# Performance work log

Hardware: AMD Instinct MI355X
Metric: run time of the kernel (lower is better)

## Reference

```python
import jax, jax.numpy as jnp
import numpy as np

ALPHA = 0.2
BETA = 1.0
TEMPERATURE = 0.05
EPS = 1e-8  # torch cosine_similarity eps


def setup_inputs() -> dict:
    key = jax.random.key(0)
    k1, k2 = jax.random.split(key)
    B, R, D = 4096, 18, 256  # rows, segment size (1 anchor + 1 pos + 16 negs), embed dim
    features = jax.random.normal(k1, (B * R, D), dtype=jnp.float32)
    scores = jax.random.normal(k2, (B * (R - 1),), dtype=jnp.float32)
    row_sizes = jnp.full((B,), R, dtype=jnp.int32)  # uniform ragged sizes
    logit_scale = jnp.array([1.0 / TEMPERATURE], dtype=jnp.float32)
    return {"features": features, "scores": scores, "row_sizes": row_sizes,
            "logit_scale": logit_scale}


def reference(features, scores, row_sizes, logit_scale):
    B = row_sizes.shape[0]
    R = features.shape[0] // B  # uniform segment size
    D = features.shape[1]
    f3 = features.reshape(B, R, D)
    anchor = f3[:, 0]          # [B, D]
    tgt = f3[:, 1:]            # [B, R-1, D]  (positive first, then negatives)

    # --- per-row cosine sims + log_softmax + KLDiv(batchmean) ---
    an = jnp.maximum(jnp.linalg.norm(anchor, axis=-1, keepdims=True), EPS)  # [B,1]
    tn = jnp.maximum(jnp.linalg.norm(tgt, axis=-1), EPS)                    # [B,R-1]
    cos = jnp.einsum('bd,bkd->bk', anchor, tgt) / (an * tn)                 # [B,R-1]
    emb_log = jax.nn.log_softmax(cos, axis=-1)                              # [B,R-1]
    ce = jax.nn.softmax(scores.reshape(B, R - 1), axis=-1)                  # [B,R-1]
    # torch KLDivLoss(reduction='batchmean') on a length-(R-1) vector divides by (R-1)
    kl = jnp.sum(ce * (jnp.log(ce) - emb_log), axis=-1) / (R - 1)           # [B]
    loss = jnp.mean(BETA * kl)

    # --- single InfoNCE over all rows: anchors vs [positives; all negatives] ---
    pos = f3[:, 1]                                   # [B, D]
    negs = f3[:, 2:].reshape(B * (R - 2), D)         # [B*(R-2), D]
    targets = jnp.concatenate([pos, negs], axis=0)   # [B*(R-1), D]
    logits = logit_scale[0] * (anchor @ targets.T)   # [B, B*(R-1)]
    labels = jnp.arange(B)
    # cross_entropy(logits, labels) with mean reduction
    infonce = jnp.mean(jax.nn.logsumexp(logits, axis=-1) - logits[labels, labels])

    return loss + ALPHA * infonce
```

## Files before the change

### kernel.cpp

```cpp
#include <hip/hip_runtime.h>
#include <math.h>

#define ALPHA 0.2f
#define BETA 1.0f
#define EPSV 1e-8f
#define LOG2E 1.4426950408889634f
#define LN2 0.6931471805599453f

#define BATCH 4096
#define RR 18
#define KT 17
#define DD 256
#define NTGT (BATCH*KT)
#define NTILE (NTGT/32)
#define TILE_BYTES (32*DD)

#define AG 16
#define NSPLIT 32
#define TPS (NTILE/NSPLIT)
#define NRING 4

#define EXPA 8388608.0f
#define EXPB 1064880320.0f

typedef int   i32x8  __attribute__((ext_vector_type(8)));
typedef float f32x16 __attribute__((ext_vector_type(16)));

__device__ inline void gl_lds16(const void* g, void* l){
  __builtin_amdgcn_global_load_lds(
      (const __attribute__((address_space(1))) unsigned int*)g,
      (__attribute__((address_space(3))) unsigned int*)l, 16, 0, 0);
}

__device__ inline int pk8(float a, float b, float c, float d){
  int p = __builtin_amdgcn_cvt_pk_fp8_f32(a, b, 0, false);
  return  __builtin_amdgcn_cvt_pk_fp8_f32(c, d, p, true);
}

__device__ inline float fmax3(float a, float b, float c){
  return fmaxf(fmaxf(a, b), c);
}

__device__ inline float fexp2u(float x, float kc){
  float t = fmaf(x, EXPA, kc);
  unsigned u;
  asm("v_cvt_u32_f32 %0, %1" : "=v"(u) : "v"(t));
  return __uint_as_float(u);
}


__global__ __launch_bounds__(256) void prep_kernel(
    const float* __restrict__ feat, const float* __restrict__ scores,
    const float* __restrict__ lscale,
    unsigned char* __restrict__ abf8, unsigned char* __restrict__ tbf8,
    float* __restrict__ diag, float* __restrict__ klarr,
    float* __restrict__ out){
  __shared__ float csh[KT];
  int b = blockIdx.x, tid = threadIdx.x;
  int grp = tid >> 4, j = tid & 15;
  const float* fb = feat + (size_t)b * RR * DD;
  float s2 = lscale[0] * LOG2E;

  if (b == 0 && tid == 0) out[0] = 0.f;

  float4 a0 = ((const float4*)fb)[j*4+0];
  float4 a1 = ((const float4*)fb)[j*4+1];
  float4 a2 = ((const float4*)fb)[j*4+2];
  float4 a3 = ((const float4*)fb)[j*4+3];
  float asq = (a0.x*a0.x+a0.y*a0.y+a0.z*a0.z+a0.w*a0.w)
            + (a1.x*a1.x+a1.y*a1.y+a1.z*a1.z+a1.w*a1.w)
            + (a2.x*a2.x+a2.y*a2.y+a2.z*a2.z+a2.w*a2.w)
            + (a3.x*a3.x+a3.y*a3.y+a3.z*a3.z+a3.w*a3.w);
  #pragma unroll
  for (int off=1; off<16; off<<=1) asq += __shfl_xor(asq, off);
  float an = fmaxf(sqrtf(asq), EPSV);

  if (tid < 16){
    uint4 v = make_uint4(
      (unsigned)pk8(a0.x*s2,a0.y*s2,a0.z*s2,a0.w*s2),
      (unsigned)pk8(a1.x*s2,a1.y*s2,a1.z*s2,a1.w*s2),
      (unsigned)pk8(a2.x*s2,a2.y*s2,a2.z*s2,a2.w*s2),
      (unsigned)pk8(a3.x*s2,a3.y*s2,a3.z*s2,a3.w*s2));
    *(uint4*)(abf8 + (size_t)b*DD + j*16) = v;
  }

  for (int kr = grp+1; kr <= KT; kr += 16){
    const float4* tp = (const float4*)(fb + (size_t)kr*DD) + j*4;
    float4 t0=tp[0], t1=tp[1], t2=tp[2], t3=tp[3];
    int t  = b*KT + (kr-1);
    int tile = t >> 5, m = t & 31;
    int ki = j >> 2, hf = (j >> 1) & 1, w = j & 1;
    uint4 v = make_uint4(
      (unsigned)pk8(t0.x,t0.y,t0.z,t0.w), (unsigned)pk8(t1.x,t1.y,t1.z,t1.w),
      (unsigned)pk8(t2.x,t2.y,t2.z,t2.w), (unsigned)pk8(t3.x,t3.y,t3.z,t3.w));
    *(uint4*)(tbf8 + (size_t)tile*TILE_BYTES + ki*2048 + w*1024 + hf*512 + m*16) = v;
    float d = (a0.x*t0.x+a0.y*t0.y+a0.z*t0.z+a0.w*t0.w)
            + (a1.x*t1.x+a1.y*t1.y+a1.z*t1.z+a1.w*t1.w)
            + (a2.x*t2.x+a2.y*t2.y+a2.z*t2.z+a2.w*t2.w)
            + (a3.x*t3.x+a3.y*t3.y+a3.z*t3.z+a3.w*t3.w);
    float q = (t0.x*t0.x+t0.y*t0.y+t0.z*t0.z+t0.w*t0.w)
            + (t1.x*t1.x+t1.y*t1.y+t1.z*t1.z+t1.w*t1.w)
            + (t2.x*t2.x+t2.y*t2.y+t2.z*t2.z+t2.w*t2.w)
            + (t3.x*t3.x+t3.y*t3.y+t3.z*t3.z+t3.w*t3.w);
    #pragma unroll
    for (int off=1; off<16; off<<=1){ d += __shfl_xor(d,off); q += __shfl_xor(q,off); }
    if (j == 0){
      csh[kr-1] = d / (an * fmaxf(sqrtf(q), EPSV));
      if (kr == 1) diag[b] = d;
    }
  }
  __syncthreads();

  if (tid < 64){
    bool act = tid < KT;
    float c  = act ? csh[tid] : -INFINITY;
    float sv = act ? scores[(size_t)b*KT + tid] : -INFINITY;
    float cm = c, sm = sv;
    #pragma unroll
    for (int off=1; off<64; off<<=1){
      cm = fmaxf(cm, __shfl_xor(cm, off));
      sm = fmaxf(sm, __shfl_xor(sm, off));
    }
    float ec = act ? __builtin_amdgcn_exp2f((c -cm)*LOG2E) : 0.f;
    float es = act ? __builtin_amdgcn_exp2f((sv-sm)*LOG2E) : 0.f;
    float cs = ec, ss = es;
    #pragma unroll
    for (int off=1; off<64; off<<=1){
      cs += __shfl_xor(cs, off);
      ss += __shfl_xor(ss, off);
    }
    float lse_c = cm + __logf(cs);
    float lse_s = sm + __logf(ss);
    float kt = 0.f;
    if (act){
      float lq = sv - lse_s;
      float lp = c  - lse_c;
      kt = __builtin_amdgcn_exp2f(lq*LOG2E)*(lq - lp);
    }
    #pragma unroll
    for (int off=1; off<64; off<<=1) kt += __shfl_xor(kt, off);
    if (tid == 0) klarr[b] = kt * (1.0f/KT);
  }
}

__global__ __launch_bounds__(256,2) void gemm_lse_kernel(
    const unsigned char* __restrict__ abf8, const unsigned char* __restrict__ tbf8,
    float* __restrict__ part_m, float* __restrict__ part_s){
  __shared__ __align__(16) unsigned char Bs[NRING][TILE_BYTES];
  const int bid  = blockIdx.x;
  const int ns   = (bid & 7)*4 + ((bid >> 3) & 3);
  const int ag   = bid >> 5;
  const int tid  = threadIdx.x;
  const int lane = tid & 63;
  const int wave = tid >> 6;
  const int l31  = lane & 31;
  const int half = lane >> 5;

  const unsigned char* gbase = tbf8 + (size_t)(ns*TPS)*TILE_BYTES;
  auto stage = [&](int t){
    const unsigned char* g = gbase + (size_t)t*TILE_BYTES;
    unsigned char* l = &Bs[t & (NRING-1)][0];
    #pragma unroll
    for (int jj=0;jj<2;++jj){
      int off = jj*4096 + tid*16;
      gl_lds16(g + off, l + off);
    }
  };

  stage(0);
  stage(1);

  i32x8 af[2][4];
  {
    const unsigned char* ab = abf8 + (size_t)(ag*256 + wave*64)*DD;
    #pragma unroll
    for (int nt=0;nt<2;++nt)
      #pragma unroll
      for (int ki=0;ki<4;++ki){
        const unsigned char* p = ab + (size_t)(nt*32+l31)*DD + ki*64 + half*32;
        uint4 lo = *(const uint4*)p;
        uint4 hi = *(const uint4*)(p+16);
        af[nt][ki] = (i32x8){(int)lo.x,(int)lo.y,(int)lo.z,(int)lo.w,
                             (int)hi.x,(int)hi.y,(int)hi.z,(int)hi.w};
      }
  }

  float run_m[2] = {-INFINITY,-INFINITY};
  float run_s[2] = {0.f,0.f};
  f32x16 accA[2], accB[2];
  #pragma unroll
  for (int nt=0;nt<2;++nt){ accA[nt]=(f32x16)(0.f); accB[nt]=(f32x16)(0.f); }

  auto mfma_tile = [&](int t, f32x16 (&acc)[2], bool last){
    if (last) asm volatile("s_waitcnt vmcnt(0)" ::: "memory");
    else      asm volatile("s_waitcnt vmcnt(2)" ::: "memory");
    __builtin_amdgcn_s_barrier();
    asm volatile("" ::: "memory");
    if (t+2 < TPS) stage(t+2);

    const unsigned char* fb = &Bs[t & (NRING-1)][0] + half*512 + l31*16;
    i32x8 tf[4];
    #pragma unroll
    for (int ki=0;ki<4;++ki){
      uint4 lo = *(const uint4*)(fb + ki*2048);
      uint4 hi = *(const uint4*)(fb + ki*2048 + 1024);
      tf[ki] = (i32x8){(int)lo.x,(int)lo.y,(int)lo.z,(int)lo.w,
                       (int)hi.x,(int)hi.y,(int)hi.z,(int)hi.w};
    }
    __builtin_amdgcn_s_setprio(1);
    #pragma unroll
    for (int ki=0;ki<4;++ki){
      acc[0] = __builtin_amdgcn_mfma_scale_f32_32x32x64_f8f6f4(
                   tf[ki], af[0][ki], acc[0], 0,0, 0,127, 0,127);
      acc[1] = __builtin_amdgcn_mfma_scale_f32_32x32x64_f8f6f4(
                   tf[ki], af[1][ki], acc[1], 0,0, 0,127, 0,127);
    }
    __builtin_amdgcn_s_setprio(0);
  };

  auto epilogue = [&](f32x16 (&acc)[2]){
    #pragma unroll
    for (int nt=0;nt<2;++nt){
      f32x16 t = acc[nt];
      float x0 = fmax3(t[0], t[1], t[2]);
      float x1 = fmax3(t[3], t[4], t[5]);
      float x2 = fmax3(t[6], t[7], t[8]);
      float x3 = fmax3(t[9], t[10], t[11]);
      float x4 = fmax3(t[12], t[13], t[14]);
      float mx = fmaxf(fmax3(x0,x1,x2), fmax3(x3,x4,t[15]));

      float kc = fmaf(mx, -EXPA, EXPB);
      float s0=0.f, s1=0.f, s2=0.f, s3=0.f;
      #pragma unroll
      for (int r=0;r<16;r+=4){
        s0 += fexp2u(t[r  ],kc);
        s1 += fexp2u(t[r+1],kc);
        s2 += fexp2u(t[r+2],kc);
        s3 += fexp2u(t[r+3],kc);
      }
      float sh = (s0+s1)+(s2+s3);

      float nm = fmaxf(run_m[nt], mx);
      run_s[nt] = run_s[nt]*__builtin_amdgcn_exp2f(run_m[nt]-nm)
                + sh*__builtin_amdgcn_exp2f(mx-nm);
      run_m[nt] = nm;
      acc[nt] = (f32x16)(0.f);
    }
  };

  mfma_tile(0, accA, false);
  for (int t=1; t+1 < TPS; t+=2){
    mfma_tile(t,   accB, false);
    epilogue(accA);
    mfma_tile(t+1, accA, false);
    epilogue(accB);
  }
  mfma_tile(TPS-1, accB, true);
  epilogue(accA);
  epilogue(accB);

  #pragma unroll
  for (int nt=0;nt<2;++nt){
    float om = __shfl_xor(run_m[nt], 32);
    float os = __shfl_xor(run_s[nt], 32);
    float nm = fmaxf(run_m[nt], om);
    float S  = run_s[nt]*__builtin_amdgcn_exp2f(run_m[nt]-nm)
             + os*__builtin_amdgcn_exp2f(om-nm);
    if (half == 0){
      int gm = ag*256 + wave*64 + nt*32 + l31;
      part_m[(size_t)ns*BATCH + gm] = nm;
      part_s[(size_t)ns*BATCH + gm] = S;
    }
  }
}

__global__ __launch_bounds__(256) void combine_kernel(
    const float* __restrict__ part_m, const float* __restrict__ part_s,
    const float* __restrict__ diag, const float* __restrict__ klarr,
    const float* __restrict__ lscale, float* __restrict__ out){
  int tid = threadIdx.x;
  int b = blockIdx.x*256 + tid;
  float s = lscale[0];
  float m = -INFINITY, S = 0.f;
  #pragma unroll
  for (int ns=0; ns<NSPLIT; ++ns){
    float pm_ = part_m[(size_t)ns*BATCH + b];
    float ps_ = part_s[(size_t)ns*BATCH + b];
    float nm = fmaxf(m, pm_);
    S = S*__builtin_amdgcn_exp2f(m-nm) + ps_*__builtin_amdgcn_exp2f(pm_-nm);
    m = nm;
  }
  float inf = (m + __log2f(S))*LN2 - s*diag[b];
  float c = BETA*klarr[b] + ALPHA*inf;
  #pragma unroll
  for (int off=1; off<64; off<<=1) c += __shfl_xor(c, off);
  if ((tid & 63) == 0) atomicAdd(out, c*(1.0f/BATCH));
}

extern "C" void kernel_launch(void* const* d_in, const int* in_sizes, int n_in,
                              void* d_out, int out_size, void* d_ws, size_t ws_size,
                              hipStream_t stream){
  const float* feat   = (const float*)d_in[0];
  const float* scores = (const float*)d_in[1];
  const float* lscale = (const float*)d_in[3];

  float* ws     = (float*)d_ws;
  float* diag   = ws;
  float* klarr  = diag + BATCH;
  float* part_m = klarr + BATCH;
  float* part_s = part_m + (size_t)NSPLIT*BATCH;
  unsigned char* abf8 = (unsigned char*)(part_s + (size_t)NSPLIT*BATCH);
  unsigned char* tbf8 = abf8 + (size_t)BATCH*DD;

  float* outp = (float*)d_out;
  prep_kernel<<<BATCH, 256, 0, stream>>>(feat, scores, lscale, abf8, tbf8,
                                         diag, klarr, outp);
  gemm_lse_kernel<<<AG*NSPLIT, 256, 0, stream>>>(abf8, tbf8, part_m, part_s);
  combine_kernel<<<BATCH/256, 256, 0, stream>>>(part_m, part_s, diag, klarr,
                                                lscale, outp);
}
```

Measured before the change: 188.0 us.

## Double-tile phases with deeper LDS ring and interleaved MFMA/exp scheduling

Restructures the GEMM+LSE main loop to process two tiles per barrier phase with an 8-deep LDS ring, halving barriers and prefetching two phases ahead. Uses sched_group_barrier to interleave the epilogue VALU work with the MFMAs. The exp-bit trick now uses packed FMA, and the online-softmax update uses a single exp2 with a select. This raises LDS usage and relies on the compiler honouring the schedule hints.

```diff
diff --git a/kernel.cpp b/kernel.cpp
--- a/kernel.cpp
+++ b/kernel.cpp
@@ -18,13 +18,17 @@
 #define AG 16
 #define NSPLIT 32
 #define TPS (NTILE/NSPLIT)
-#define NRING 4
+#define PHASES (TPS/2)
+#define NRING 8
 
 #define EXPA 8388608.0f
 #define EXPB 1064880320.0f
 
 typedef int   i32x8  __attribute__((ext_vector_type(8)));
 typedef float f32x16 __attribute__((ext_vector_type(16)));
+typedef float f32x2  __attribute__((ext_vector_type(2)));
+
+#define SGB __builtin_amdgcn_sched_group_barrier
 
 __device__ inline void gl_lds16(const void* g, void* l){
   __builtin_amdgcn_global_load_lds(
@@ -41,10 +45,15 @@
   return fmaxf(fmaxf(a, b), c);
 }
 
-__device__ inline float fexp2u(float x, float kc){
-  float t = fmaf(x, EXPA, kc);
+__device__ inline f32x2 pk_fma2(f32x2 a, f32x2 b, f32x2 c){
+  f32x2 d;
+  asm("v_pk_fma_f32 %0, %1, %2, %3" : "=v"(d) : "v"(a), "v"(b), "v"(c));
+  return d;
+}
+
+__device__ inline float cvtbit(float x){
   unsigned u;
-  asm("v_cvt_u32_f32 %0, %1" : "=v"(u) : "v"(t));
+  asm("v_cvt_u32_f32 %0, %1" : "=v"(u) : "v"(x));
   return __uint_as_float(u);
 }
 
@@ -157,18 +166,16 @@
   const int half = lane >> 5;
 
   const unsigned char* gbase = tbf8 + (size_t)(ns*TPS)*TILE_BYTES;
-  auto stage = [&](int t){
+  auto stage_tile = [&](int t){
     const unsigned char* g = gbase + (size_t)t*TILE_BYTES;
     unsigned char* l = &Bs[t & (NRING-1)][0];
-    #pragma unroll
-    for (int jj=0;jj<2;++jj){
-      int off = jj*4096 + tid*16;
-      gl_lds16(g + off, l + off);
-    }
+    gl_lds16(g + tid*16,        l + tid*16);
+    gl_lds16(g + 4096 + tid*16, l + 4096 + tid*16);
   };
-
-  stage(0);
-  stage(1);
+  auto stage_phase = [&](int p){ stage_tile(2*p); stage_tile(2*p+1); };
+
+  stage_phase(0);
+  stage_phase(1);
 
   i32x8 af[2][4];
   {
@@ -188,16 +195,9 @@
   float run_m[2] = {-INFINITY,-INFINITY};
   float run_s[2] = {0.f,0.f};
   f32x16 accA[2], accB[2];
-  #pragma unroll
-  for (int nt=0;nt<2;++nt){ accA[nt]=(f32x16)(0.f); accB[nt]=(f32x16)(0.f); }
-
-  auto mfma_tile = [&](int t, f32x16 (&acc)[2], bool last){
-    if (last) asm volatile("s_waitcnt vmcnt(0)" ::: "memory");
-    else      asm volatile("s_waitcnt vmcnt(2)" ::: "memory");
-    __builtin_amdgcn_s_barrier();
-    asm volatile("" ::: "memory");
-    if (t+2 < TPS) stage(t+2);
-
+  f32x2 A2; A2[0]=EXPA; A2[1]=EXPA;
+
+  auto tile_mfma = [&](int t, f32x16 (&acc)[2]){
     const unsigned char* fb = &Bs[t & (NRING-1)][0] + half*512 + l31*16;
     i32x8 tf[4];
     #pragma unroll
@@ -207,7 +207,8 @@
       tf[ki] = (i32x8){(int)lo.x,(int)lo.y,(int)lo.z,(int)lo.w,
                        (int)hi.x,(int)hi.y,(int)hi.z,(int)hi.w};
     }
-    __builtin_amdgcn_s_setprio(1);
+    acc[0] = (f32x16)(0.f);
+    acc[1] = (f32x16)(0.f);
     #pragma unroll
     for (int ki=0;ki<4;++ki){
       acc[0] = __builtin_amdgcn_mfma_scale_f32_32x32x64_f8f6f4(
@@ -215,7 +216,6 @@
       acc[1] = __builtin_amdgcn_mfma_scale_f32_32x32x64_f8f6f4(
                    tf[ki], af[1][ki], acc[1], 0,0, 0,127, 0,127);
     }
-    __builtin_amdgcn_s_setprio(0);
   };
 
   auto epilogue = [&](f32x16 (&acc)[2]){
@@ -230,33 +230,56 @@
       float mx = fmaxf(fmax3(x0,x1,x2), fmax3(x3,x4,t[15]));
 
       float kc = fmaf(mx, -EXPA, EXPB);
+      f32x2 kc2; kc2[0]=kc; kc2[1]=kc;
       float s0=0.f, s1=0.f, s2=0.f, s3=0.f;
       #pragma unroll
       for (int r=0;r<16;r+=4){
-        s0 += fexp2u(t[r  ],kc);
-        s1 += fexp2u(t[r+1],kc);
-        s2 += fexp2u(t[r+2],kc);
-        s3 += fexp2u(t[r+3],kc);
+        f32x2 p0; p0[0]=t[r];   p0[1]=t[r+1];
+        f32x2 p1; p1[0]=t[r+2]; p1[1]=t[r+3];
+        f32x2 e0 = pk_fma2(p0, A2, kc2);
+        f32x2 e1 = pk_fma2(p1, A2, kc2);
+        s0 += cvtbit(e0[0]); s1 += cvtbit(e0[1]);
+        s2 += cvtbit(e1[0]); s3 += cvtbit(e1[1]);
       }
       float sh = (s0+s1)+(s2+s3);
 
-      float nm = fmaxf(run_m[nt], mx);
-      run_s[nt] = run_s[nt]*__builtin_amdgcn_exp2f(run_m[nt]-nm)
-                + sh*__builtin_amdgcn_exp2f(mx-nm);
-      run_m[nt] = nm;
-      acc[nt] = (f32x16)(0.f);
+      float d = mx - run_m[nt];
+      float e = __builtin_amdgcn_exp2f(-fabsf(d));
+      bool g  = d > 0.f;
+      run_s[nt] = g ? fmaf(run_s[nt], e, sh) : fmaf(sh, e, run_s[nt]);
+      run_m[nt] = g ? mx : run_m[nt];
     }
   };
 
-  mfma_tile(0, accA, false);
-  for (int t=1; t+1 < TPS; t+=2){
-    mfma_tile(t,   accB, false);
+  auto sched_mix = [&](){
+    SGB(0x100, 8, 0);
+    SGB(0x002, 24, 0);
+    #pragma unroll
+    for (int i=0;i<8;++i){ SGB(0x008, 1, 0); SGB(0x002, 11, 0); }
+  };
+
+  asm volatile("s_waitcnt vmcnt(4)" ::: "memory");
+  __builtin_amdgcn_s_barrier();
+  stage_phase(2);
+  tile_mfma(0, accA);
+  tile_mfma(1, accB);
+  epilogue(accA);
+
+  for (int p = 1; p < PHASES; ++p){
+    if (p < PHASES-1) asm volatile("s_waitcnt vmcnt(4)" ::: "memory");
+    else              asm volatile("s_waitcnt vmcnt(0)" ::: "memory");
+    __builtin_amdgcn_s_barrier();
+    asm volatile("" ::: "memory");
+    if (p+2 < PHASES) stage_phase(p+2);
+
+    tile_mfma(2*p, accA);
+    epilogue(accB);
+    sched_mix();
+
+    tile_mfma(2*p+1, accB);
     epilogue(accA);
-    mfma_tile(t+1, accA, false);
-    epilogue(accB);
-  }
-  mfma_tile(TPS-1, accB, true);
-  epilogue(accA);
+    sched_mix();
+  }
   epilogue(accB);
 
   #pragma unroll
```

After: 190.4 us. No clear change (+1.3%).
